# Kernel optimization log

Hardware: AMD Instinct MI355X
Metric: run time of the kernel (lower is better)

## Reference

```python
import jax, jax.numpy as jnp
import numpy as np

B, Q, K, D, U = 8, 128, 512, 256, 256  # batch, q_len, kv_len, feat dim, units
NEG_INF = -1e6


def setup_inputs() -> dict:
    key = jax.random.key(0)
    ks = jax.random.split(key, 7)
    query = jax.random.normal(ks[0], (B, Q, D), dtype=jnp.float32)
    k_in = jax.random.normal(ks[1], (B, K, D), dtype=jnp.float32)
    value = jax.random.normal(ks[2], (B, K, D), dtype=jnp.float32)
    valid_len = jax.random.randint(ks[3], (B,), 1, K + 1, dtype=jnp.int32)
    s = 1.0 / np.sqrt(D)
    Wq = jax.random.uniform(ks[4], (D, U), jnp.float32, -s, s)
    Wk = jax.random.uniform(ks[5], (D, U), jnp.float32, -s, s)
    v_w = jax.random.uniform(ks[6], (U,), jnp.float32, -1.0 / np.sqrt(U), 1.0 / np.sqrt(U))
    return {"query": query, "key": k_in, "value": value, "valid_len": valid_len,
            "Wq": Wq, "Wk": Wk, "v_w": v_w}


def reference(query, key, value, valid_len, Wq, Wk, v_w):
    # projections: [B,Q,U] and [B,K,U]
    q = jnp.einsum('bqd,du->bqu', query, Wq)
    k = jnp.einsum('bkd,du->bku', key, Wk)
    # additive features [B,Q,K,U] -> tanh -> reduce with v: scores [B,Q,K]
    feats = jnp.tanh(q[:, :, None, :] + k[:, None, :, :])
    scores = jnp.einsum('bqku,u->bqk', feats, v_w)
    # masked softmax over keys: positions >= valid_len[b] masked out
    mask = jnp.arange(K)[None, None, :] < valid_len[:, None, None]
    scores = jnp.where(mask, scores, NEG_INF)
    attn = jax.nn.softmax(scores, axis=-1)
    # dropout p=0.0 (eval) -> identity
    return jnp.einsum('bqk,bkd->bqd', attn, value)
```

## Files before the change

### kernel.cpp

```cpp
#include <hip/hip_runtime.h>
#include <hip/hip_bf16.h>

#ifndef __has_builtin
#define __has_builtin(x) 0
#endif

__device__ __forceinline__ float fast_exp2(float x) {
#if __has_builtin(__builtin_amdgcn_exp2f)
  return __builtin_amdgcn_exp2f(x);
#else
  return exp2f(x);
#endif
}
__device__ __forceinline__ float fast_rcp(float x) {
#if __has_builtin(__builtin_amdgcn_rcpf)
  return __builtin_amdgcn_rcpf(x);
#else
  return 1.0f / x;
#endif
}

constexpr int Bsz = 8, QL = 128, KL = 512, DD = 256, UU = 256;
constexpr int PR = 4;
constexpr int DT = 8;
constexpr float NEG_INF = -1e6f;
constexpr float C2 = 2.885390081777927f;

__global__ __launch_bounds__(256) void proj_kernel(
    const float* __restrict__ query, const float* __restrict__ key,
    const float* __restrict__ Wq, const float* __restrict__ Wk,
    const int* __restrict__ valid_len,
    float* __restrict__ qp, float* __restrict__ kpT)
{
  const int u   = threadIdx.x;
  const int blk = blockIdx.x;

  constexpr int QBLKS = Bsz * QL / PR;
  const bool isQ = blk < QBLKS;
  const int  m0  = isQ ? blk * PR : (blk - QBLKS) * PR;

  const int kb_b = m0 / KL, kb_k0 = m0 % KL;
  if (!isQ) {
    if (kb_k0 >= valid_len[kb_b]) return;
  }
  const float* __restrict__ in = isQ ? query : key;
  const float* __restrict__ W  = isQ ? Wq : Wk;
  const float* r0 = in + (size_t)m0 * DD;

  float acc[PR];
#pragma unroll
  for (int r = 0; r < PR; ++r) acc[r] = 0.f;

  float  w_c[DT], w_n[DT];
  float4 r_c[PR][2], r_n[PR][2];

#pragma unroll
  for (int j = 0; j < DT; ++j) w_c[j] = W[j * UU + u];
#pragma unroll
  for (int r = 0; r < PR; ++r) {
    r_c[r][0] = *reinterpret_cast<const float4*>(r0 + r * DD);
    r_c[r][1] = *reinterpret_cast<const float4*>(r0 + r * DD + 4);
  }

  for (int d = 0; d < DD; d += DT) {
    const int dn = (d + DT < DD) ? d + DT : 0;
#pragma unroll
    for (int j = 0; j < DT; ++j) w_n[j] = W[(dn + j) * UU + u];
#pragma unroll
    for (int r = 0; r < PR; ++r) {
      r_n[r][0] = *reinterpret_cast<const float4*>(r0 + r * DD + dn);
      r_n[r][1] = *reinterpret_cast<const float4*>(r0 + r * DD + dn + 4);
    }
#pragma unroll
    for (int r = 0; r < PR; ++r) {
      float a = acc[r];
      a = fmaf(r_c[r][0].x, w_c[0], a);
      a = fmaf(r_c[r][0].y, w_c[1], a);
      a = fmaf(r_c[r][0].z, w_c[2], a);
      a = fmaf(r_c[r][0].w, w_c[3], a);
      a = fmaf(r_c[r][1].x, w_c[4], a);
      a = fmaf(r_c[r][1].y, w_c[5], a);
      a = fmaf(r_c[r][1].z, w_c[6], a);
      a = fmaf(r_c[r][1].w, w_c[7], a);
      acc[r] = a;
    }
#pragma unroll
    for (int j = 0; j < DT; ++j) w_c[j] = w_n[j];
#pragma unroll
    for (int r = 0; r < PR; ++r) { r_c[r][0] = r_n[r][0]; r_c[r][1] = r_n[r][1]; }
  }

  if (isQ) {
    float* o = qp + (size_t)m0 * UU + u;
#pragma unroll
    for (int r = 0; r < PR; ++r) o[(size_t)r * UU] = fast_exp2(acc[r] * C2);
  } else {
    float4 cv;
    cv.x = fast_exp2(acc[0] * C2); cv.y = fast_exp2(acc[1] * C2);
    cv.z = fast_exp2(acc[2] * C2); cv.w = fast_exp2(acc[3] * C2);
    *reinterpret_cast<float4*>(kpT + ((size_t)kb_b * UU + u) * KL + kb_k0) = cv;
  }
}

__global__ __launch_bounds__(512) void fused_attn_kernel(
    const float* __restrict__ value, const int* __restrict__ valid_len,
    const float* __restrict__ v_w, const float* __restrict__ qp,
    const float* __restrict__ kpT, float* __restrict__ out)
{
  __shared__ __align__(16) float sps0[KL];
  __shared__ __align__(16) float sps1[KL];
  __shared__ float2 redM[8], redS[8];

  const int t = threadIdx.x;
  const int w = t >> 6, l = t & 63;

  const int g = blockIdx.x;
  const int x = g & 7;
  const int i = g >> 3;
  int vl[8];
#pragma unroll
  for (int bi = 0; bi < 8; ++bi) vl[bi] = valid_len[bi];
  const int rk = (i < 32) ? x : (7 - x);
  int b = 0;
#pragma unroll
  for (int bi = 0; bi < 8; ++bi) {
    int r = 0;
#pragma unroll
    for (int bj = 0; bj < 8; ++bj)
      r += (vl[bj] > vl[bi]) || (vl[bj] == vl[bi] && bj < bi);
    if (r == rk) b = bi;
  }
  const int vlen = vl[b];
  const int qq = i;
  const int q0 = qq * 2;

  const int s  = (w + qq) & 7;
  const int kb = 64 * s + l;

  const float* __restrict__ qrow0 = qp + (size_t)(b * QL + q0) * UU;
  const float* __restrict__ qrow1 = qrow0 + UU;

  float a0 = 0.f, a1 = 0.f;
  if (64 * s < vlen) {
    const float* __restrict__ kcol = kpT + (size_t)b * UU * KL + kb;
    float c[8], n[8];
#pragma unroll
    for (int j = 0; j < 8; ++j) c[j] = kcol[(size_t)j * KL];

    for (int u0 = 0; u0 < UU; u0 += 8) {
      const int un = (u0 + 8 < UU) ? u0 + 8 : 0;
#pragma unroll
      for (int j = 0; j < 8; ++j) n[j] = kcol[(size_t)(un + j) * KL];
#pragma unroll
      for (int j = 0; j < 8; ++j) {
        const float Eq0 = qrow0[u0 + j];
        const float Eq1 = qrow1[u0 + j];
        const float wv  = v_w[u0 + j];
        const float d0 = fmaf(Eq0, c[j], 1.0f);
        const float d1 = fmaf(Eq1, c[j], 1.0f);
        a0 = fmaf(wv, fast_rcp(d0), a0);
        a1 = fmaf(wv, fast_rcp(d1), a1);
      }
#pragma unroll
      for (int j = 0; j < 8; ++j) c[j] = n[j];
    }
  }
  const float s0 = (kb < vlen) ? -(a0 + a0) : NEG_INF;
  const float s1 = (kb < vlen) ? -(a1 + a1) : NEG_INF;

  float mx0 = s0, mx1 = s1;
#pragma unroll
  for (int off = 32; off >= 1; off >>= 1) {
    mx0 = fmaxf(mx0, __shfl_xor(mx0, off, 64));
    mx1 = fmaxf(mx1, __shfl_xor(mx1, off, 64));
  }
  if (l == 0) redM[w] = make_float2(mx0, mx1);
  __syncthreads();
  float m0 = redM[0].x, m1 = redM[0].y;
#pragma unroll
  for (int j = 1; j < 8; ++j) {
    m0 = fmaxf(m0, redM[j].x);
    m1 = fmaxf(m1, redM[j].y);
  }

  const float e0 = __expf(s0 - m0);
  const float e1 = __expf(s1 - m1);
  sps0[kb] = e0;
  sps1[kb] = e1;
  float ss0 = e0, ss1 = e1;
#pragma unroll
  for (int off = 32; off >= 1; off >>= 1) {
    ss0 += __shfl_xor(ss0, off, 64);
    ss1 += __shfl_xor(ss1, off, 64);
  }
  if (l == 0) redS[w] = make_float2(ss0, ss1);
  __syncthreads();
  float sum0 = redS[0].x, sum1 = redS[0].y;
#pragma unroll
  for (int j = 1; j < 8; ++j) {
    sum0 += redS[j].x;
    sum1 += redS[j].y;
  }
  const float inv0 = fast_rcp(sum0);
  const float inv1 = fast_rcp(sum1);

  const int   r2 = t >> 8;
  const int   d  = t & 255;
  const float* __restrict__ sp = r2 ? sps1 : sps0;
  const float  inv = r2 ? inv1 : inv0;
  const float* __restrict__ vb = value + (size_t)b * KL * DD + d;
  const int kmax = (vlen + 15) & ~15;

  float o = 0.f;
  float vc[16], vn[16];
#pragma unroll
  for (int j = 0; j < 16; ++j) vc[j] = vb[(size_t)j * DD];
  for (int k = 0; k < kmax; k += 16) {
    const int kn = (k + 16 < kmax) ? k + 16 : 0;
#pragma unroll
    for (int j = 0; j < 16; ++j) vn[j] = vb[(size_t)(kn + j) * DD];
    const float4* __restrict__ sp4 =
        reinterpret_cast<const float4*>(sp + k);
    const float4 p0 = sp4[0], p1 = sp4[1], p2 = sp4[2], p3 = sp4[3];
    o = fmaf(p0.x, vc[0],  o); o = fmaf(p0.y, vc[1],  o);
    o = fmaf(p0.z, vc[2],  o); o = fmaf(p0.w, vc[3],  o);
    o = fmaf(p1.x, vc[4],  o); o = fmaf(p1.y, vc[5],  o);
    o = fmaf(p1.z, vc[6],  o); o = fmaf(p1.w, vc[7],  o);
    o = fmaf(p2.x, vc[8],  o); o = fmaf(p2.y, vc[9],  o);
    o = fmaf(p2.z, vc[10], o); o = fmaf(p2.w, vc[11], o);
    o = fmaf(p3.x, vc[12], o); o = fmaf(p3.y, vc[13], o);
    o = fmaf(p3.z, vc[14], o); o = fmaf(p3.w, vc[15], o);
#pragma unroll
    for (int j = 0; j < 16; ++j) vc[j] = vn[j];
  }
  out[(size_t)(b * QL + q0 + r2) * DD + d] = o * inv;
}

extern "C" void kernel_launch(void* const* d_in, const int* in_sizes, int n_in,
                              void* d_out, int out_size, void* d_ws, size_t ws_size,
                              hipStream_t stream) {
  const float* query     = (const float*)d_in[0];
  const float* key       = (const float*)d_in[1];
  const float* value     = (const float*)d_in[2];
  const int*   valid_len = (const int*)d_in[3];
  const float* Wq        = (const float*)d_in[4];
  const float* Wk        = (const float*)d_in[5];
  const float* v_w       = (const float*)d_in[6];
  float* out = (float*)d_out;

  float* qp  = (float*)d_ws;
  float* kpT = qp + (size_t)Bsz * QL * UU;

  const int proj_blocks = (Bsz * QL + Bsz * KL) / PR;
  proj_kernel<<<proj_blocks, 256, 0, stream>>>(query, key, Wq, Wk, valid_len,
                                               qp, kpT);

  const int fused_blocks = Bsz * QL / 2;
  fused_attn_kernel<<<fused_blocks, 512, 0, stream>>>(value, valid_len, v_w,
                                                      qp, kpT, out);
}
```

Baseline: 117.9 us.

## Split score reduction over U across warps and balance PV over key halves

The score phase now gives each warp a 32-wide slice of the unit dimension and loops over only the valid 64-key chunks, so all warps share the work for valid keys instead of whole warps idling on masked chunks. Per-warp partial scores are summed through shared memory, and q/v_w are packed into LDS as float4. The PV phase splits the key range into two halves per thread group, each computing both query rows, and combines them through shared memory. This is meant to remove load imbalance from variable valid_len, at the cost of more shared memory (about 27KB), extra syncs and partial-sum traffic.

Measured after the change: 113.3 us. 1.04x faster.

```diff
diff --git a/kernel.cpp b/kernel.cpp
--- a/kernel.cpp
+++ b/kernel.cpp
@@ -107,8 +107,11 @@
     const float* __restrict__ v_w, const float* __restrict__ qp,
     const float* __restrict__ kpT, float* __restrict__ out)
 {
-  __shared__ __align__(16) float sps0[KL];
-  __shared__ __align__(16) float sps1[KL];
+  __shared__ __align__(16) float4 qpack[UU];
+  __shared__ __align__(16) float2 sp_part[8][8][64];
+  __shared__ __align__(16) float  sps0[KL];
+  __shared__ __align__(16) float  sps1[KL];
+  __shared__ __align__(16) float2 opart[DD];
   __shared__ float2 redM[8], redS[8];
 
   const int t = threadIdx.x;
@@ -131,42 +134,55 @@
     if (r == rk) b = bi;
   }
   const int vlen = vl[b];
-  const int qq = i;
-  const int q0 = qq * 2;
-
-  const int s  = (w + qq) & 7;
-  const int kb = 64 * s + l;
-
-  const float* __restrict__ qrow0 = qp + (size_t)(b * QL + q0) * UU;
-  const float* __restrict__ qrow1 = qrow0 + UU;
-
-  float a0 = 0.f, a1 = 0.f;
-  if (64 * s < vlen) {
-    const float* __restrict__ kcol = kpT + (size_t)b * UU * KL + kb;
-    float c[8], n[8];
-#pragma unroll
-    for (int j = 0; j < 8; ++j) c[j] = kcol[(size_t)j * KL];
-
-    for (int u0 = 0; u0 < UU; u0 += 8) {
-      const int un = (u0 + 8 < UU) ? u0 + 8 : 0;
-#pragma unroll
-      for (int j = 0; j < 8; ++j) n[j] = kcol[(size_t)(un + j) * KL];
-#pragma unroll
-      for (int j = 0; j < 8; ++j) {
-        const float Eq0 = qrow0[u0 + j];
-        const float Eq1 = qrow1[u0 + j];
-        const float wv  = v_w[u0 + j];
-        const float d0 = fmaf(Eq0, c[j], 1.0f);
-        const float d1 = fmaf(Eq1, c[j], 1.0f);
-        a0 = fmaf(wv, fast_rcp(d0), a0);
-        a1 = fmaf(wv, fast_rcp(d1), a1);
+  const int q0 = i * 2;
+  const int nc = (vlen + 63) >> 6;
+
+  if (t < UU) {
+    qpack[t] = make_float4(qp[(size_t)(b * QL + q0) * UU + t],
+                           qp[(size_t)(b * QL + q0 + 1) * UU + t],
+                           v_w[t], 0.f);
+  }
+  __syncthreads();
+
+  {
+    const float* __restrict__ kbase =
+        kpT + ((size_t)(b * UU) + 32 * w) * KL + l;
+    for (int c = 0; c < nc; ++c) {
+      const int k64 = 64 * c;
+      float a0 = 0.f, a1 = 0.f;
+      float cb[8], nb[8];
+#pragma unroll
+      for (int j = 0; j < 8; ++j) cb[j] = kbase[(size_t)j * KL + k64];
+#pragma unroll 1
+      for (int ug = 0; ug < 32; ug += 8) {
+        const int un = (ug + 8 < 32) ? ug + 8 : 0;
+#pragma unroll
+        for (int j = 0; j < 8; ++j) nb[j] = kbase[(size_t)(un + j) * KL + k64];
+#pragma unroll
+        for (int j = 0; j < 8; ++j) {
+          const float4 qv = qpack[32 * w + ug + j];
+          const float d0 = fmaf(qv.x, cb[j], 1.0f);
+          const float d1 = fmaf(qv.y, cb[j], 1.0f);
+          a0 = fmaf(qv.z, fast_rcp(d0), a0);
+          a1 = fmaf(qv.z, fast_rcp(d1), a1);
+        }
+#pragma unroll
+        for (int j = 0; j < 8; ++j) cb[j] = nb[j];
       }
-#pragma unroll
-      for (int j = 0; j < 8; ++j) c[j] = n[j];
-    }
-  }
-  const float s0 = (kb < vlen) ? -(a0 + a0) : NEG_INF;
-  const float s1 = (kb < vlen) ? -(a1 + a1) : NEG_INF;
+      sp_part[w][c][l] = make_float2(a0, a1);
+    }
+  }
+  __syncthreads();
+
+  float s0 = 0.f, s1 = 0.f;
+#pragma unroll
+  for (int ws = 0; ws < 8; ++ws) {
+    const float2 p = sp_part[ws][w][l];
+    s0 += p.x; s1 += p.y;
+  }
+  const int key = t;
+  s0 = (key < vlen) ? -(s0 + s0) : NEG_INF;
+  s1 = (key < vlen) ? -(s1 + s1) : NEG_INF;
 
   float mx0 = s0, mx1 = s1;
 #pragma unroll
@@ -185,8 +201,8 @@
 
   const float e0 = __expf(s0 - m0);
   const float e1 = __expf(s1 - m1);
-  sps0[kb] = e0;
-  sps1[kb] = e1;
+  sps0[key] = e0;
+  sps1[key] = e1;
   float ss0 = e0, ss1 = e1;
 #pragma unroll
   for (int off = 32; off >= 1; off >>= 1) {
@@ -204,36 +220,54 @@
   const float inv0 = fast_rcp(sum0);
   const float inv1 = fast_rcp(sum1);
 
-  const int   r2 = t >> 8;
-  const int   d  = t & 255;
-  const float* __restrict__ sp = r2 ? sps1 : sps0;
-  const float  inv = r2 ? inv1 : inv0;
-  const float* __restrict__ vb = value + (size_t)b * KL * DD + d;
-  const int kmax = (vlen + 15) & ~15;
-
-  float o = 0.f;
-  float vc[16], vn[16];
-#pragma unroll
-  for (int j = 0; j < 16; ++j) vc[j] = vb[(size_t)j * DD];
-  for (int k = 0; k < kmax; k += 16) {
-    const int kn = (k + 16 < kmax) ? k + 16 : 0;
-#pragma unroll
-    for (int j = 0; j < 16; ++j) vn[j] = vb[(size_t)(kn + j) * DD];
-    const float4* __restrict__ sp4 =
-        reinterpret_cast<const float4*>(sp + k);
-    const float4 p0 = sp4[0], p1 = sp4[1], p2 = sp4[2], p3 = sp4[3];
-    o = fmaf(p0.x, vc[0],  o); o = fmaf(p0.y, vc[1],  o);
-    o = fmaf(p0.z, vc[2],  o); o = fmaf(p0.w, vc[3],  o);
-    o = fmaf(p1.x, vc[4],  o); o = fmaf(p1.y, vc[5],  o);
-    o = fmaf(p1.z, vc[6],  o); o = fmaf(p1.w, vc[7],  o);
-    o = fmaf(p2.x, vc[8],  o); o = fmaf(p2.y, vc[9],  o);
-    o = fmaf(p2.z, vc[10], o); o = fmaf(p2.w, vc[11], o);
-    o = fmaf(p3.x, vc[12], o); o = fmaf(p3.y, vc[13], o);
-    o = fmaf(p3.z, vc[14], o); o = fmaf(p3.w, vc[15], o);
-#pragma unroll
-    for (int j = 0; j < 16; ++j) vc[j] = vn[j];
-  }
-  out[(size_t)(b * QL + q0 + r2) * DD + d] = o * inv;
+  const int h = t >> 8, d = t & 255;
+  const int kmax  = (vlen + 15) & ~15;
+  const int khalf = ((kmax >> 1) + 15) & ~15;
+  const int kst = h ? khalf : 0;
+  const int ken = h ? kmax : khalf;
+
+  float o0 = 0.f, o1 = 0.f;
+  if (ken > kst) {
+    const float* __restrict__ vb = value + (size_t)b * KL * DD + d;
+    float vc[16], vn[16];
+#pragma unroll
+    for (int j = 0; j < 16; ++j) vc[j] = vb[(size_t)(kst + j) * DD];
+#pragma unroll 1
+    for (int k = kst; k < ken; k += 16) {
+      const int kn = (k + 16 < ken) ? k + 16 : kst;
+#pragma unroll
+      for (int j = 0; j < 16; ++j) vn[j] = vb[(size_t)(kn + j) * DD];
+      const float4* __restrict__ p4 = reinterpret_cast<const float4*>(sps0 + k);
+      const float4* __restrict__ q4 = reinterpret_cast<const float4*>(sps1 + k);
+      const float4 p0 = p4[0], p1 = p4[1], p2 = p4[2], p3 = p4[3];
+      const float4 r0 = q4[0], r1 = q4[1], r2 = q4[2], r3 = q4[3];
+      o0 = fmaf(p0.x, vc[0],  o0); o1 = fmaf(r0.x, vc[0],  o1);
+      o0 = fmaf(p0.y, vc[1],  o0); o1 = fmaf(r0.y, vc[1],  o1);
+      o0 = fmaf(p0.z, vc[2],  o0); o1 = fmaf(r0.z, vc[2],  o1);
+      o0 = fmaf(p0.w, vc[3],  o0); o1 = fmaf(r0.w, vc[3],  o1);
+      o0 = fmaf(p1.x, vc[4],  o0); o1 = fmaf(r1.x, vc[4],  o1);
+      o0 = fmaf(p1.y, vc[5],  o0); o1 = fmaf(r1.y, vc[5],  o1);
+      o0 = fmaf(p1.z, vc[6],  o0); o1 = fmaf(r1.z, vc[6],  o1);
+      o0 = fmaf(p1.w, vc[7],  o0); o1 = fmaf(r1.w, vc[7],  o1);
+      o0 = fmaf(p2.x, vc[8],  o0); o1 = fmaf(r2.x, vc[8],  o1);
+      o0 = fmaf(p2.y, vc[9],  o0); o1 = fmaf(r2.y, vc[9],  o1);
+      o0 = fmaf(p2.z, vc[10], o0); o1 = fmaf(r2.z, vc[10], o1);
+      o0 = fmaf(p2.w, vc[11], o0); o1 = fmaf(r2.w, vc[11], o1);
+      o0 = fmaf(p3.x, vc[12], o0); o1 = fmaf(r3.x, vc[12], o1);
+      o0 = fmaf(p3.y, vc[13], o0); o1 = fmaf(r3.y, vc[13], o1);
+      o0 = fmaf(p3.z, vc[14], o0); o1 = fmaf(r3.z, vc[14], o1);
+      o0 = fmaf(p3.w, vc[15], o0); o1 = fmaf(r3.w, vc[15], o1);
+#pragma unroll
+      for (int j = 0; j < 16; ++j) vc[j] = vn[j];
+    }
+  }
+  if (h) opart[d] = make_float2(o0, o1);
+  __syncthreads();
+  if (!h) {
+    const float2 p = opart[d];
+    out[(size_t)(b * QL + q0) * DD + d]     = (o0 + p.x) * inv0;
+    out[(size_t)(b * QL + q0 + 1) * DD + d] = (o1 + p.y) * inv1;
+  }
 }
 
 extern "C" void kernel_launch(void* const* d_in, const int* in_sizes, int n_in,
```
